# Kernel optimization log

Hardware: AMD Instinct MI355X
Metric: run time of the kernel (lower is better)

The kernel has to match this reference:

```python
import jax, jax.numpy as jnp
import numpy as np

N_VERT = 1000          # num_of_vertices; x has 3*N_VERT rows
B = 32                 # batch
IN_DIM = 64
OUT_DIMS = [64, 64, 64]


def setup_inputs() -> dict:
    key = jax.random.key(0)
    ks = jax.random.split(key, 8)
    threeN = 3 * N_VERT
    x = jax.random.normal(ks[0], (threeN, B, IN_DIM), dtype=jnp.float32)
    # dense (normalized-ish) adjacency over the localized spatio-temporal graph
    adj = jax.random.uniform(ks[1], (threeN, threeN), dtype=jnp.float32) / threeN
    inp = {"x": x, "adj": adj}
    in_d = IN_DIM
    for i, out_d in enumerate(OUT_DIMS):
        # torch Linear(in_d, 2*out_d): store as [in_d, 2*out_d] for x @ W + b
        scale = 1.0 / np.sqrt(in_d)
        inp[f"W{i}"] = jax.random.uniform(ks[2 + 2 * i], (in_d, 2 * out_d),
                                          minval=-scale, maxval=scale, dtype=jnp.float32)
        inp[f"b{i}"] = jax.random.uniform(ks[3 + 2 * i], (2 * out_d,),
                                          minval=-scale, maxval=scale, dtype=jnp.float32)
        in_d = out_d
    return inp


def _gcn_glu(adj, x, W, b, out_dim):
    # aggregate: [3N,3N] x [3N,B,C] -> [3N,B,C]
    h = jnp.einsum('nm,mbc->nbc', adj, x)
    lr = h @ W + b                       # [3N,B,2*out]
    lhs, rhs = lr[..., :out_dim], lr[..., out_dim:]
    return lhs * jax.nn.sigmoid(rhs)     # GLU


def reference(x, adj, W0, b0, W1, b1, W2, b2):
    n = x.shape[0] // 3
    Ws = [(W0, b0), (W1, b1), (W2, b2)]
    mids = []
    h = x
    for (W, b), out_d in zip(Ws, OUT_DIMS):
        h = _gcn_glu(adj, h, W, b, out_d)
        mids.append(h[n:2 * n])          # middle time-step slice [N,B,out]
    return jnp.max(jnp.stack(mids, axis=0), axis=0)  # [N,B,out]
```

## Files before the change

### kernel.cpp

```cpp
#include <hip/hip_runtime.h>
#include <stdint.h>
#include <math.h>

#define NV   3000
#define MP   3072
#define NBC  2048
#define NMID 1000

typedef unsigned short u16;
typedef short  s8vec __attribute__((ext_vector_type(8)));
typedef float  f4vec __attribute__((ext_vector_type(4)));


__device__ __forceinline__ u16 f2b(float f) {
  union { float f; unsigned int u; } v; v.f = f;
  unsigned int r = v.u + 0x7FFFu + ((v.u >> 16) & 1u);
  return (u16)(r >> 16);
}
__device__ __forceinline__ float b2f(u16 u) {
  union { unsigned int u; float f; } v; v.u = ((unsigned int)u) << 16;
  return v.f;
}

__device__ __forceinline__ void gload16(const void* g, void* l) {
  __builtin_amdgcn_global_load_lds(
      (const __attribute__((address_space(1))) void*)g,
      (__attribute__((address_space(3))) void*)l, 16, 0, 0);
}

__global__ void k_conv_adj(const float* __restrict__ adj,
                           u16* __restrict__ adjt) {
  __shared__ __align__(16) u16 tb[64][80];
  const int bx = blockIdx.x;
  const int by = blockIdx.y;
  const int t  = threadIdx.x;

  {
    const int rl = t >> 2, quad = t & 3;
    const int r  = by * 64 + rl;
    const bool rok = (r < NV);
#pragma unroll
    for (int i = 0; i < 4; ++i) {
      int c = bx * 64 + quad * 16 + i * 4;
      float4 f = {0.f, 0.f, 0.f, 0.f};
      if (rok && c < NV) f = *(const float4*)(adj + (size_t)r * NV + c);
      ushort4 o;
      o.x = f2b(f.x); o.y = f2b(f.y); o.z = f2b(f.z); o.w = f2b(f.w);
      *(ushort4*)&tb[rl][quad * 16 + i * 4] = o;
    }
  }
  __syncthreads();

  {
#pragma unroll
    for (int h = 0; h < 2; ++h) {
      int chunk = t * 2 + h;
      int sel  = chunk >> 8;
      int g    = (chunk >> 6) & 3;
      int lane = chunk & 63;
      int row  = g * 16 + (lane & 15);
      int col  = sel * 32 + (lane >> 4) * 8;
      s8vec v = *(const s8vec*)&tb[row][col];
      size_t dst = ((size_t)(by * 96 + bx * 2 + sel) * 4 + g) * 512 + lane * 8;
      *(s8vec*)(adjt + dst) = v;
    }
  }
}

__global__ void k_conv_x(const float* __restrict__ x,
                         u16* __restrict__ xt) {
  __shared__ __align__(16) u16 tb[64][72];
  int t  = threadIdx.x;
  int k0 = blockIdx.x * 64;
  int n0 = blockIdx.y * 64;
  int kl = t >> 4, ch = t & 15;
#pragma unroll
  for (int r = 0; r < 4; ++r) {
    int k = k0 + kl + r * 16;
    float4 f = {0.f, 0.f, 0.f, 0.f};
    if (k < NV) f = *(const float4*)(x + (size_t)k * NBC + n0 + ch * 4);
    tb[ch * 4 + 0][kl + r * 16] = f2b(f.x);
    tb[ch * 4 + 1][kl + r * 16] = f2b(f.y);
    tb[ch * 4 + 2][kl + r * 16] = f2b(f.z);
    tb[ch * 4 + 3][kl + r * 16] = f2b(f.w);
  }
  __syncthreads();
  int nl = t >> 4, kc = t & 15;
#pragma unroll
  for (int r = 0; r < 4; ++r) {
    int n = n0 + nl + r * 16;
    int k = k0 + kc * 4;
    ushort4 o;
    o.x = tb[nl + r * 16][kc * 4 + 0];
    o.y = tb[nl + r * 16][kc * 4 + 1];
    o.z = tb[nl + r * 16][kc * 4 + 2];
    o.w = tb[nl + r * 16][kc * 4 + 3];
    int nt = n >> 7, g = (n >> 4) & 7, lr = n & 15;
    int kk = k >> 5, hi = (k >> 3) & 3, j = k & 7;
    size_t dst = ((size_t)(nt * 96 + kk) * 8 + g) * 512 +
                 (size_t)(hi * 16 + lr) * 8 + j;
    *(ushort4*)(xt + dst) = o;
  }
}

__global__ void k_conv_w(const float* __restrict__ W0,
                         const float* __restrict__ W1,
                         const float* __restrict__ W2,
                         u16* __restrict__ Wt) {
  int e = blockIdx.x * 256 + threadIdx.x;
  const float* W = (e < 8192) ? W0 : (e < 16384) ? W1 : W2;
  int r  = e & 8191;
  int kk = r >> 12, g = (r >> 9) & 7, ln = (r >> 3) & 63, jj = r & 7;
  int c = kk * 32 + (ln >> 4) * 8 + jj;
  int j = g * 16 + (ln & 15);
  Wt[e] = f2b(W[c * 128 + j]);
}

template <int NKT>
__global__ __launch_bounds__(256, 3) void k_gemm(
    const u16* __restrict__ At,
    const u16* __restrict__ Xt,
    u16* __restrict__ Cbase,
    size_t cslot,
    int mtbase,
    int nmt,
    int crow0,
    int chunk) {
  __shared__ __align__(16) u16 S[3 * 8192];

  const int bid = blockIdx.x;
  const int swz = (bid & 7) * chunk + (bid >> 3);
  const int nt  = swz & 15;
  const int mk  = swz >> 4;
  const int ks  = mk / nmt;
  const int mt  = mk - ks * nmt;
  const int kt0 = ks * NKT;

  const int tid  = threadIdx.x;
  const int w    = tid >> 6;
  const int lane = tid & 63;
  const int wr   = w >> 1;
  const int wc   = w & 1;

  const int c0 = w * 4;
  const u16* src[4];
  int stp[4];
#pragma unroll
  for (int i = 0; i < 4; ++i) {
    int c = c0 + i;
    if (c < 8) {
      int m64 = (mtbase + mt) * 2 + (c >> 2);
      src[i] = At + ((size_t)(m64 * 96 + kt0) * 4 + (c & 3)) * 512 + lane * 8;
      stp[i] = 2048;
    } else {
      src[i] = Xt + ((size_t)(nt * 96 + kt0) * 8 + (c - 8)) * 512 + lane * 8;
      stp[i] = 4096;
    }
  }

  f4vec acc[4][4];
#pragma unroll
  for (int i = 0; i < 4; ++i)
#pragma unroll
    for (int j = 0; j < 4; ++j) acc[i][j] = (f4vec){0.f, 0.f, 0.f, 0.f};

  auto stage = [&](int buf, int s) {
    u16* d = S + buf * 8192 + c0 * 512;
#pragma unroll
    for (int i = 0; i < 4; ++i)
      gload16(src[i] + (size_t)s * stp[i], d + i * 512);
  };
  auto compute = [&](int buf) {
    const u16* Ab = S + buf * 8192 + (wr * 4) * 512 + lane * 8;
    const u16* Bb = S + buf * 8192 + 4096 + (wc * 4) * 512 + lane * 8;
    s8vec a[4], b[4];
#pragma unroll
    for (int mi = 0; mi < 4; ++mi)
      a[mi] = *(const s8vec*)(Ab + mi * 512);
#pragma unroll
    for (int ni = 0; ni < 4; ++ni)
      b[ni] = *(const s8vec*)(Bb + ni * 512);
    __builtin_amdgcn_s_setprio(1);
#pragma unroll
    for (int mi = 0; mi < 4; ++mi)
#pragma unroll
      for (int ni = 0; ni < 4; ++ni)
        acc[mi][ni] = __builtin_amdgcn_mfma_f32_16x16x32_bf16(
            a[mi], b[ni], acc[mi][ni], 0, 0, 0);
    __builtin_amdgcn_s_setprio(0);
  };

  stage(0, 0);
  stage(1, 1);

#pragma unroll 1
  for (int sb = 0; sb < NKT - 3; sb += 3) {
#pragma unroll
    for (int u = 0; u < 3; ++u) {
      const int s = sb + u;
      asm volatile("s_waitcnt vmcnt(4)" ::: "memory");
      asm volatile("s_barrier" ::: "memory");
      stage((u + 2) % 3, s + 2);
      compute(u);
    }
  }
  asm volatile("s_waitcnt vmcnt(4)" ::: "memory");
  asm volatile("s_barrier" ::: "memory");
  stage(2, NKT - 1);
  compute(0);
  asm volatile("s_waitcnt vmcnt(4)" ::: "memory");
  asm volatile("s_barrier" ::: "memory");
  compute(1);
  asm volatile("s_waitcnt vmcnt(0)" ::: "memory");
  asm volatile("s_barrier" ::: "memory");
  compute(2);

  u16* Cs = Cbase + (size_t)ks * cslot;
  const int rl = lane & 15;
  const int rh = lane >> 4;
  const int mrow0 = (mtbase + mt) * 128 + wr * 64 - crow0;
#pragma unroll
  for (int mi = 0; mi < 4; ++mi)
#pragma unroll
    for (int ni = 0; ni < 4; ++ni) {
      int grow = mrow0 + mi * 16 + rh * 4;
      int gcol = nt * 128 + wc * 64 + ni * 16 + rl;
      u16* cp = Cs + (size_t)grow * NBC + gcol;
      cp[0 * NBC] = f2b(acc[mi][ni][0]);
      cp[1 * NBC] = f2b(acc[mi][ni][1]);
      cp[2 * NBC] = f2b(acc[mi][ni][2]);
      cp[3 * NBC] = f2b(acc[mi][ni][3]);
    }
}

template <int LAYER0, int WRITEX, int NH>
__global__ __launch_bounds__(256) void k_layerB(
    const u16* __restrict__ H0,
    const u16* __restrict__ H1,
    const u16* __restrict__ H2,
    const u16* __restrict__ H3,
    const u16* __restrict__ Wt,
    const float* __restrict__ bias,
    u16* __restrict__ xt,
    float* __restrict__ out,
    int vt0) {
  __shared__ __align__(16) u16 Hs[NH][2][8][64][8];

  const u16* Hp[4] = {H0, H1, H2, H3};
  const int vt = vt0 + blockIdx.x;
  const int b  = blockIdx.y;
  const int v0 = vt * 128;
  const int t  = threadIdx.x;

#pragma unroll
  for (int h = 0; h < NH; ++h) {
    const u16* H = Hp[h];
#pragma unroll
    for (int q = 0; q < 4; ++q) {
      int id = q * 256 + t;
      int v  = id >> 3;
      int cc = (id & 7) * 8;
      s8vec hh = *(const s8vec*)(H + (size_t)(v0 + v) * NBC + b * 64 + cc);
      int kk = cc >> 5, g = v >> 4, ln = ((cc >> 3) & 3) * 16 + (v & 15);
      *(s8vec*)&Hs[h][kk][g][ln][0] = hh;
    }
  }
  __syncthreads();

  const int w    = t >> 6;
  const int lane = t & 63;
  const int wvh  = w >> 1;
  const int wc   = w & 1;

  s8vec bf[4][2];
#pragma unroll
  for (int ni = 0; ni < 4; ++ni) {
    int g = (ni < 2) ? (wc * 2 + ni) : (4 + wc * 2 + (ni - 2));
#pragma unroll
    for (int kk = 0; kk < 2; ++kk)
      bf[ni][kk] = *(const s8vec*)(Wt + ((size_t)(kk * 8 + g) * 64 + lane) * 8);
  }

  f4vec acc[4][4];
#pragma unroll
  for (int i = 0; i < 4; ++i)
#pragma unroll
    for (int j = 0; j < 4; ++j) acc[i][j] = (f4vec){0.f, 0.f, 0.f, 0.f};

#pragma unroll
  for (int h = 0; h < NH; ++h)
#pragma unroll
    for (int kk = 0; kk < 2; ++kk) {
      s8vec a[4];
#pragma unroll
      for (int mi = 0; mi < 4; ++mi)
        a[mi] = *(const s8vec*)&Hs[h][kk][wvh * 4 + mi][lane][0];
#pragma unroll
      for (int mi = 0; mi < 4; ++mi)
#pragma unroll
        for (int ni = 0; ni < 4; ++ni)
          acc[mi][ni] = __builtin_amdgcn_mfma_f32_16x16x32_bf16(
              a[mi], bf[ni][kk], acc[mi][ni], 0, 0, 0);
    }

  const int lr = lane & 15;
  const int rh = lane >> 4;
#pragma unroll
  for (int mi = 0; mi < 4; ++mi) {
    const int vbase = v0 + wvh * 64 + mi * 16 + rh * 4;
#pragma unroll
    for (int np = 0; np < 2; ++np) {
      const int j  = wc * 32 + np * 16 + lr;
      const float bl = bias[j];
      const float bh = bias[j + 64];
      float vals[4];
#pragma unroll
      for (int r = 0; r < 4; ++r) {
        float lo = acc[mi][np][r] + bl;
        float hi = acc[mi][np + 2][r] + bh;
        float gv = lo / (1.0f + __expf(-hi));
        vals[r] = ((vbase + r) < NV) ? gv : 0.0f;
      }
#pragma unroll
      for (int r = 0; r < 4; ++r) {
        int vg = vbase + r;
        if (vg >= NMID && vg < 2 * NMID) {
          size_t oi = (size_t)(vg - NMID) * NBC + b * 64 + j;
          if (LAYER0) out[oi] = vals[r];
          else        out[oi] = fmaxf(out[oi], vals[r]);
        }
      }
      if (WRITEX) {
        int n   = b * 64 + j;
        int nt  = n >> 7, g2 = (n >> 4) & 7, ln2 = n & 15;
        int kk2 = vbase >> 5, hi2 = (vbase >> 3) & 3, jj0 = vbase & 7;
        ushort4 o;
        o.x = f2b(vals[0]); o.y = f2b(vals[1]);
        o.z = f2b(vals[2]); o.w = f2b(vals[3]);
        size_t dst = ((size_t)(nt * 96 + kk2) * 8 + g2) * 512 +
                     (size_t)(hi2 * 16 + ln2) * 8 + jj0;
        *(ushort4*)(xt + dst) = o;
      }
    }
  }
}

extern "C" void kernel_launch(void* const* d_in, const int* in_sizes, int n_in,
                              void* d_out, int out_size, void* d_ws, size_t ws_size,
                              hipStream_t stream) {
  const float* x   = (const float*)d_in[0];
  const float* adj = (const float*)d_in[1];
  const float* W0  = (const float*)d_in[2];
  const float* b0  = (const float*)d_in[3];
  const float* W1  = (const float*)d_in[4];
  const float* b1  = (const float*)d_in[5];
  const float* W2  = (const float*)d_in[6];
  const float* b2  = (const float*)d_in[7];
  float* out = (float*)d_out;

  char* ws = (char*)d_ws;
  u16* adjt = (u16*)ws;
  u16* xa   = (u16*)(ws + 18874368);
  u16* Hbuf = (u16*)(ws + 18874368 + 12582912);
  u16* Wt   = (u16*)(ws + 18874368 + 12582912 + 25165824);

  const size_t FS = (size_t)3072 * NBC;
  const size_t QS = (size_t)1536 * NBC;
  const size_t R0 = (size_t)512 * NBC;

  k_conv_adj<<<dim3(48, 48), 256, 0, stream>>>(adj, adjt);
  k_conv_x<<<dim3(48, 32), 256, 0, stream>>>(x, xa);
  k_conv_w<<<96, 256, 0, stream>>>(W0, W1, W2, Wt);

  k_gemm<48><<<768, 256, 0, stream>>>(adjt, xa, Hbuf, FS, 0, 24, 0, 96);
  k_layerB<1, 1, 2><<<dim3(24, 32), 256, 0, stream>>>(
      Hbuf, Hbuf + FS, Hbuf, Hbuf, Wt, b0, xa, out, 0);
  k_gemm<48><<<768, 256, 0, stream>>>(adjt, xa, Hbuf, FS, 0, 24, 0, 96);
  k_layerB<0, 1, 2><<<dim3(24, 32), 256, 0, stream>>>(
      Hbuf, Hbuf + FS, Hbuf, Hbuf, Wt + 8192, b1, xa, out, 0);
  k_gemm<24><<<768, 256, 0, stream>>>(adjt, xa, Hbuf, QS, 4, 12, 512, 96);
  k_layerB<0, 0, 4><<<dim3(9, 32), 256, 0, stream>>>(
      Hbuf - R0, Hbuf + QS - R0, Hbuf + 2 * QS - R0, Hbuf + 3 * QS - R0,
      Wt + 16384, b2, xa, out, 7);
}
```

Before: 180.3 us.

## Merge conversion kernels and use a two-way K split for the last layer

The three fp32-to-bf16 conversion kernels are merged into one launch that dispatches on block index, which removes two launch overheads. The third-layer GEMM now computes only 9 middle row tiles with a 2-way K split (288 blocks, NKT=48) instead of 12 tiles with a 4-way split (768 blocks, NKT=24). The final layer kernel therefore sums two partial buffers instead of four, which cuts partial-result write and read traffic and reduces wasted rows. The cost is fewer blocks in the last GEMM, which may leave the GPU underutilised.

```diff
diff --git a/kernel.cpp b/kernel.cpp
--- a/kernel.cpp
+++ b/kernel.cpp
@@ -28,92 +28,91 @@
       (__attribute__((address_space(3))) void*)l, 16, 0, 0);
 }
 
-__global__ void k_conv_adj(const float* __restrict__ adj,
-                           u16* __restrict__ adjt) {
+__global__ void k_conv(const float* __restrict__ adj,
+                       const float* __restrict__ x,
+                       const float* __restrict__ W0,
+                       const float* __restrict__ W1,
+                       const float* __restrict__ W2,
+                       u16* __restrict__ adjt,
+                       u16* __restrict__ xt,
+                       u16* __restrict__ Wt) {
   __shared__ __align__(16) u16 tb[64][80];
-  const int bx = blockIdx.x;
-  const int by = blockIdx.y;
-  const int t  = threadIdx.x;
-
-  {
-    const int rl = t >> 2, quad = t & 3;
-    const int r  = by * 64 + rl;
-    const bool rok = (r < NV);
-#pragma unroll
-    for (int i = 0; i < 4; ++i) {
-      int c = bx * 64 + quad * 16 + i * 4;
+  const int bid = blockIdx.x;
+  const int t   = threadIdx.x;
+
+  if (bid < 2304) {
+    const int bx = bid % 48;
+    const int by = bid / 48;
+    {
+      const int rl = t >> 2, quad = t & 3;
+      const int r  = by * 64 + rl;
+      const bool rok = (r < NV);
+#pragma unroll
+      for (int i = 0; i < 4; ++i) {
+        int c = bx * 64 + quad * 16 + i * 4;
+        float4 f = {0.f, 0.f, 0.f, 0.f};
+        if (rok && c < NV) f = *(const float4*)(adj + (size_t)r * NV + c);
+        ushort4 o;
+        o.x = f2b(f.x); o.y = f2b(f.y); o.z = f2b(f.z); o.w = f2b(f.w);
+        *(ushort4*)&tb[rl][quad * 16 + i * 4] = o;
+      }
+    }
+    __syncthreads();
+    {
+#pragma unroll
+      for (int h = 0; h < 2; ++h) {
+        int chunk = t * 2 + h;
+        int sel  = chunk >> 8;
+        int g    = (chunk >> 6) & 3;
+        int lane = chunk & 63;
+        int row  = g * 16 + (lane & 15);
+        int col  = sel * 32 + (lane >> 4) * 8;
+        s8vec v = *(const s8vec*)&tb[row][col];
+        size_t dst = ((size_t)(by * 96 + bx * 2 + sel) * 4 + g) * 512 + lane * 8;
+        *(s8vec*)(adjt + dst) = v;
+      }
+    }
+  } else if (bid < 3840) {
+    const int r2 = bid - 2304;
+    const int k0 = (r2 % 48) * 64;
+    const int n0 = (r2 / 48) * 64;
+    int kl = t >> 4, ch = t & 15;
+#pragma unroll
+    for (int r = 0; r < 4; ++r) {
+      int k = k0 + kl + r * 16;
       float4 f = {0.f, 0.f, 0.f, 0.f};
-      if (rok && c < NV) f = *(const float4*)(adj + (size_t)r * NV + c);
+      if (k < NV) f = *(const float4*)(x + (size_t)k * NBC + n0 + ch * 4);
+      tb[ch * 4 + 0][kl + r * 16] = f2b(f.x);
+      tb[ch * 4 + 1][kl + r * 16] = f2b(f.y);
+      tb[ch * 4 + 2][kl + r * 16] = f2b(f.z);
+      tb[ch * 4 + 3][kl + r * 16] = f2b(f.w);
+    }
+    __syncthreads();
+    int nl = t >> 4, kc = t & 15;
+#pragma unroll
+    for (int r = 0; r < 4; ++r) {
+      int n = n0 + nl + r * 16;
+      int k = k0 + kc * 4;
       ushort4 o;
-      o.x = f2b(f.x); o.y = f2b(f.y); o.z = f2b(f.z); o.w = f2b(f.w);
-      *(ushort4*)&tb[rl][quad * 16 + i * 4] = o;
-    }
-  }
-  __syncthreads();
-
-  {
-#pragma unroll
-    for (int h = 0; h < 2; ++h) {
-      int chunk = t * 2 + h;
-      int sel  = chunk >> 8;
-      int g    = (chunk >> 6) & 3;
-      int lane = chunk & 63;
-      int row  = g * 16 + (lane & 15);
-      int col  = sel * 32 + (lane >> 4) * 8;
-      s8vec v = *(const s8vec*)&tb[row][col];
-      size_t dst = ((size_t)(by * 96 + bx * 2 + sel) * 4 + g) * 512 + lane * 8;
-      *(s8vec*)(adjt + dst) = v;
-    }
-  }
-}
-
-__global__ void k_conv_x(const float* __restrict__ x,
-                         u16* __restrict__ xt) {
-  __shared__ __align__(16) u16 tb[64][72];
-  int t  = threadIdx.x;
-  int k0 = blockIdx.x * 64;
-  int n0 = blockIdx.y * 64;
-  int kl = t >> 4, ch = t & 15;
-#pragma unroll
-  for (int r = 0; r < 4; ++r) {
-    int k = k0 + kl + r * 16;
-    float4 f = {0.f, 0.f, 0.f, 0.f};
-    if (k < NV) f = *(const float4*)(x + (size_t)k * NBC + n0 + ch * 4);
-    tb[ch * 4 + 0][kl + r * 16] = f2b(f.x);
-    tb[ch * 4 + 1][kl + r * 16] = f2b(f.y);
-    tb[ch * 4 + 2][kl + r * 16] = f2b(f.z);
-    tb[ch * 4 + 3][kl + r * 16] = f2b(f.w);
-  }
-  __syncthreads();
-  int nl = t >> 4, kc = t & 15;
-#pragma unroll
-  for (int r = 0; r < 4; ++r) {
-    int n = n0 + nl + r * 16;
-    int k = k0 + kc * 4;
-    ushort4 o;
-    o.x = tb[nl + r * 16][kc * 4 + 0];
-    o.y = tb[nl + r * 16][kc * 4 + 1];
-    o.z = tb[nl + r * 16][kc * 4 + 2];
-    o.w = tb[nl + r * 16][kc * 4 + 3];
-    int nt = n >> 7, g = (n >> 4) & 7, lr = n & 15;
-    int kk = k >> 5, hi = (k >> 3) & 3, j = k & 7;
-    size_t dst = ((size_t)(nt * 96 + kk) * 8 + g) * 512 +
-                 (size_t)(hi * 16 + lr) * 8 + j;
-    *(ushort4*)(xt + dst) = o;
-  }
-}
-
-__global__ void k_conv_w(const float* __restrict__ W0,
-                         const float* __restrict__ W1,
-                         const float* __restrict__ W2,
-                         u16* __restrict__ Wt) {
-  int e = blockIdx.x * 256 + threadIdx.x;
-  const float* W = (e < 8192) ? W0 : (e < 16384) ? W1 : W2;
-  int r  = e & 8191;
-  int kk = r >> 12, g = (r >> 9) & 7, ln = (r >> 3) & 63, jj = r & 7;
-  int c = kk * 32 + (ln >> 4) * 8 + jj;
-  int j = g * 16 + (ln & 15);
-  Wt[e] = f2b(W[c * 128 + j]);
+      o.x = tb[nl + r * 16][kc * 4 + 0];
+      o.y = tb[nl + r * 16][kc * 4 + 1];
+      o.z = tb[nl + r * 16][kc * 4 + 2];
+      o.w = tb[nl + r * 16][kc * 4 + 3];
+      int nt = n >> 7, g = (n >> 4) & 7, lr = n & 15;
+      int kk = k >> 5, hi = (k >> 3) & 3, j = k & 7;
+      size_t dst = ((size_t)(nt * 96 + kk) * 8 + g) * 512 +
+                   (size_t)(hi * 16 + lr) * 8 + j;
+      *(ushort4*)(xt + dst) = o;
+    }
+  } else {
+    int e = (bid - 3840) * 256 + t;
+    const float* W = (e < 8192) ? W0 : (e < 16384) ? W1 : W2;
+    int r  = e & 8191;
+    int kk = r >> 12, g = (r >> 9) & 7, ln = (r >> 3) & 63, jj = r & 7;
+    int c = kk * 32 + (ln >> 4) * 8 + jj;
+    int j = g * 16 + (ln & 15);
+    Wt[e] = f2b(W[c * 128 + j]);
+  }
 }
 
 template <int NKT>
@@ -233,28 +232,25 @@
     }
 }
 
-template <int LAYER0, int WRITEX, int NH>
+template <int LAYER0, int WRITEX>
 __global__ __launch_bounds__(256) void k_layerB(
     const u16* __restrict__ H0,
     const u16* __restrict__ H1,
-    const u16* __restrict__ H2,
-    const u16* __restrict__ H3,
     const u16* __restrict__ Wt,
     const float* __restrict__ bias,
     u16* __restrict__ xt,
     float* __restrict__ out,
     int vt0) {
-  __shared__ __align__(16) u16 Hs[NH][2][8][64][8];
-
-  const u16* Hp[4] = {H0, H1, H2, H3};
+  __shared__ __align__(16) u16 Hs[2][2][8][64][8];
+
   const int vt = vt0 + blockIdx.x;
   const int b  = blockIdx.y;
   const int v0 = vt * 128;
   const int t  = threadIdx.x;
 
 #pragma unroll
-  for (int h = 0; h < NH; ++h) {
-    const u16* H = Hp[h];
+  for (int h = 0; h < 2; ++h) {
+    const u16* H = h ? H1 : H0;
 #pragma unroll
     for (int q = 0; q < 4; ++q) {
       int id = q * 256 + t;
@@ -288,7 +284,7 @@
     for (int j = 0; j < 4; ++j) acc[i][j] = (f4vec){0.f, 0.f, 0.f, 0.f};
 
 #pragma unroll
-  for (int h = 0; h < NH; ++h)
+  for (int h = 0; h < 2; ++h)
 #pragma unroll
     for (int kk = 0; kk < 2; ++kk) {
       s8vec a[4];
@@ -365,21 +361,18 @@
   u16* Wt   = (u16*)(ws + 18874368 + 12582912 + 25165824);
 
   const size_t FS = (size_t)3072 * NBC;
-  const size_t QS = (size_t)1536 * NBC;
-  const size_t R0 = (size_t)512 * NBC;
-
-  k_conv_adj<<<dim3(48, 48), 256, 0, stream>>>(adj, adjt);
-  k_conv_x<<<dim3(48, 32), 256, 0, stream>>>(x, xa);
-  k_conv_w<<<96, 256, 0, stream>>>(W0, W1, W2, Wt);
+  const size_t PS = (size_t)1152 * NBC;
+  const size_t R0 = (size_t)896 * NBC;
+
+  k_conv<<<3936, 256, 0, stream>>>(adj, x, W0, W1, W2, adjt, xa, Wt);
 
   k_gemm<48><<<768, 256, 0, stream>>>(adjt, xa, Hbuf, FS, 0, 24, 0, 96);
-  k_layerB<1, 1, 2><<<dim3(24, 32), 256, 0, stream>>>(
-      Hbuf, Hbuf + FS, Hbuf, Hbuf, Wt, b0, xa, out, 0);
+  k_layerB<1, 1><<<dim3(24, 32), 256, 0, stream>>>(
+      Hbuf, Hbuf + FS, Wt, b0, xa, out, 0);
   k_gemm<48><<<768, 256, 0, stream>>>(adjt, xa, Hbuf, FS, 0, 24, 0, 96);
-  k_layerB<0, 1, 2><<<dim3(24, 32), 256, 0, stream>>>(
-      Hbuf, Hbuf + FS, Hbuf, Hbuf, Wt + 8192, b1, xa, out, 0);
-  k_gemm<24><<<768, 256, 0, stream>>>(adjt, xa, Hbuf, QS, 4, 12, 512, 96);
-  k_layerB<0, 0, 4><<<dim3(9, 32), 256, 0, stream>>>(
-      Hbuf - R0, Hbuf + QS - R0, Hbuf + 2 * QS - R0, Hbuf + 3 * QS - R0,
-      Wt + 16384, b2, xa, out, 7);
-}
+  k_layerB<0, 1><<<dim3(24, 32), 256, 0, stream>>>(
+      Hbuf, Hbuf + FS, Wt + 8192, b1, xa, out, 0);
+  k_gemm<48><<<288, 256, 0, stream>>>(adjt, xa, Hbuf, PS, 7, 9, 896, 36);
+  k_layerB<0, 0><<<dim3(9, 32), 256, 0, stream>>>(
+      Hbuf - R0, Hbuf + PS - R0, Wt + 16384, b2, xa, out, 7);
+}
```

After: 172.6 us (median of 2 runs). -4.3%, faster.
